# Optimization experiments

Hardware: AMD Instinct MI355X
Metric: run time of the kernel (lower is better)

The kernel has to match this reference:

```python
import jax, jax.numpy as jnp
import numpy as np

N, C, NUM_IDS = 4096, 2048, 256


def setup_inputs() -> dict:
    key = jax.random.key(0)
    k1, k2 = jax.random.split(key)
    x = jax.random.normal(k1, (N, C), dtype=jnp.float32)
    target = jax.random.randint(k2, (N,), 0, NUM_IDS, dtype=jnp.int64)
    return {
        "input": x,
        "target": target,
        "hyper_paramter": 1,
        "usemean": 1,
        "use_exp": 0,
    }


def _pair_stats(x, W):
    """Vectorized sum over lower-tri pairs (i>j) weighted by W (lower-triangular 0/1).

    cov = sum_{i>j} W_ij (x_i - x_j)(x_i - x_j)^T = X^T (diag(S 1) - S) X, S = W + W^T
    vec = sum_{i>j} W_ij (x_i - x_j)       = X^T (rowsum(W) - colsum(W))
    """
    S = W + W.T                       # [N, N] symmetric pair mask
    d = S.sum(axis=1)                 # degree
    Lx = d[:, None] * x - S @ x       # (diag(d) - S) @ X, [N, C]
    cov = x.T @ Lx                    # [C, C]
    vec = x.T @ (W.sum(axis=1) - W.sum(axis=0))  # [C]
    return cov, vec, W.sum()


def reference(input, target, hyper_paramter, usemean, use_exp):
    x = input
    same_id = (target[:, None] == target[None, :])
    pos_l = jnp.tril(same_id.astype(x.dtype), -1)          # positive pairs, i>j
    neg_l = jnp.tril((~same_id).astype(x.dtype), -1)       # negative pairs, i>j

    cov_i, sum_i, npos = _pair_stats(x, pos_l)
    cov_j, sum_j, nneg = _pair_stats(x, neg_l)

    norm_i = jnp.linalg.norm(cov_i)
    norm_j = jnp.linalg.norm(cov_j)

    if use_exp:
        dist = jnp.exp(-jnp.linalg.norm(cov_i - cov_j))
        loss = dist
    else:
        # original broadcasts zeros(C) + diff(C,1) -> (C,C) matrix of identical
        # columns; its Frobenius norm = sqrt(C) * norm(column vector)
        mean_norm = jnp.sqrt(jnp.asarray(x.shape[1], x.dtype)) * jnp.linalg.norm(
            sum_i / npos - sum_j / nneg
        )
        dist = norm_i - hyper_paramter * norm_j - usemean * mean_norm
        loss = jnp.maximum(dist, 0.0)
    return (loss, dist, norm_i, norm_j)
```

## Files before the change

### kernel.cpp

```cpp
#include <hip/hip_runtime.h>
#include <math.h>


#define N_ROWS 4096
#define C_DIM  2048
#define NCLS   256
#define RLCAP  96
#define NRB    17
#define NKS    64
#define TSB    16384
#define SLOT_B 32768

typedef __attribute__((ext_vector_type(8))) short short8v;
typedef __attribute__((ext_vector_type(4))) float f32x4;

__device__ __forceinline__ unsigned short f2bf(float f) {
    unsigned u = __float_as_uint(f);
    u += 0x7FFF + ((u >> 16) & 1);
    return (unsigned short)(u >> 16);
}

__device__ __forceinline__ void gload16(const void* g, void* l) {
    __builtin_amdgcn_global_load_lds(
        (const __attribute__((address_space(1))) unsigned int*)g,
        (__attribute__((address_space(3))) unsigned int*)l, 16, 0, 0);
}

__device__ __forceinline__ int swz_off(int r, int c8) {
    return r * 64 + ((c8 ^ ((r >> 1) & 3)) << 4);
}

__global__ __launch_bounds__(256) void k_scan_conv(
    const int* __restrict__ t, const float* __restrict__ x,
    float* __restrict__ ca, float* __restrict__ cb,
    float* __restrict__ dr, float* __restrict__ nposf,
    unsigned char* __restrict__ xbf) {
    __shared__ int ts[N_ROWS];
    __shared__ int rl[RLCAP];
    __shared__ int cnt_s;
    int a = blockIdx.x, tid = threadIdx.x;
    for (int i = tid; i < N_ROWS; i += 256) ts[i] = t[i];
    __syncthreads();
    if (tid < 64) {
        int lane = tid;
        unsigned long long ltmask = (1ULL << lane) - 1ULL;
        int base = 0;
        for (int i0 = 0; i0 < N_ROWS; i0 += 64) {
            int i = i0 + lane;
            bool m = (ts[i] == a);
            unsigned long long mask = __ballot(m);
            if (m) {
                int r = base + (int)__popcll(mask & ltmask);
                if (r < RLCAP) rl[r] = i;
            }
            base += (int)__popcll(mask);
        }
        if (lane == 0) {
            cnt_s = base;
            float cf = (float)base;
            atomicAdd(nposf, 0.5f * cf * (cf - 1.f));
        }
        int cc = base < RLCAP ? base : RLCAP;
        for (int r = lane; r < cc; r += 64) {
            int i = rl[r];
            ca[i] = (float)(2 * r - base + 1);
            cb[i] = (float)(2 * i - 2 * r + base - N_ROWS);
            dr[i] = (float)base;
        }
    }
    __syncthreads();
    int cnt = cnt_s < RLCAP ? cnt_s : RLCAP;
    int c0 = tid * 4, c1 = 1024 + tid * 4;
    float s0=0,s1=0,s2=0,s3=0,s4=0,s5=0,s6=0,s7=0;
    int ks0 = c0 >> 5, c80 = (c0 & 31) >> 3, sb0 = (c0 & 4) << 1;
    int ks1 = c1 >> 5, c81 = (c1 & 31) >> 3, sb1 = (c1 & 4) << 1;
    for (int r = 0; r < cnt; ++r) {
        int i = rl[r];
        const float* row = x + (size_t)i * C_DIM;
        float4 v0 = *(const float4*)(row + c0);
        float4 v1 = *(const float4*)(row + c1);
        s0+=v0.x; s1+=v0.y; s2+=v0.z; s3+=v0.w;
        s4+=v1.x; s5+=v1.y; s6+=v1.z; s7+=v1.w;
        int rb2 = i >> 8, rr = i & 255;
        unsigned char* tb = xbf + (size_t)rb2 * NKS * TSB;
        int2 w0, w1;
        w0.x = (int)((unsigned)f2bf(v0.x) | ((unsigned)f2bf(v0.y) << 16));
        w0.y = (int)((unsigned)f2bf(v0.z) | ((unsigned)f2bf(v0.w) << 16));
        w1.x = (int)((unsigned)f2bf(v1.x) | ((unsigned)f2bf(v1.y) << 16));
        w1.y = (int)((unsigned)f2bf(v1.z) | ((unsigned)f2bf(v1.w) << 16));
        *(int2*)(tb + (size_t)ks0 * TSB + swz_off(rr, c80) + sb0) = w0;
        *(int2*)(tb + (size_t)ks1 * TSB + swz_off(rr, c81) + sb1) = w1;
    }
    unsigned char* tbg = xbf + (size_t)16 * NKS * TSB;
    int2 g0, g1;
    g0.x = (int)((unsigned)f2bf(s0) | ((unsigned)f2bf(s1) << 16));
    g0.y = (int)((unsigned)f2bf(s2) | ((unsigned)f2bf(s3) << 16));
    g1.x = (int)((unsigned)f2bf(s4) | ((unsigned)f2bf(s5) << 16));
    g1.y = (int)((unsigned)f2bf(s6) | ((unsigned)f2bf(s7) << 16));
    *(int2*)(tbg + (size_t)ks0 * TSB + swz_off(a, c80) + sb0) = g0;
    *(int2*)(tbg + (size_t)ks1 * TSB + swz_off(a, c81) + sb1) = g1;
}

__device__ __forceinline__ short8v frag64(const unsigned char* buf, int row0,
                                          int lane) {
    int r = row0 + (lane & 15);
    int c8 = lane >> 4;
    return *(const short8v*)(buf + swz_off(r, c8));
}

__global__ __launch_bounds__(1024, 4) void k_gram(
    const unsigned char* __restrict__ xbf, const float* __restrict__ dr,
    const float* __restrict__ ca, const float* __restrict__ cb,
    const float* __restrict__ nposf, float* __restrict__ ssq) {
    const int nwg = NRB * (NRB + 1) / 2;
    int orig = blockIdx.x;
    int q8 = nwg >> 3, r8 = nwg & 7;
    int xcd = orig & 7, loc = orig >> 3;
    int b = (xcd < r8 ? xcd * (q8 + 1) : r8 * (q8 + 1) + (xcd - r8) * q8) + loc;
    int bi = 0;
    while (b >= NRB - bi) { b -= NRB - bi; ++bi; }
    int bj = bi + b;
    bool diag = (bi == bj);
    bool needRS = (bj == NRB - 1);

    __shared__ __align__(16) unsigned char Sl[4][SLOT_B];
    __shared__ float drow[256], dcol[256], urow[256], ucol[256];
    __shared__ float rsum[256];
    __shared__ float wred[16 * 16];

    int tid = threadIdx.x;
    int lane = tid & 63;
    int w = tid >> 6;
    int wr4 = w >> 2;
    int wc4 = w & 3;

    const unsigned char* abase = xbf + (size_t)bi * NKS * TSB;
    const unsigned char* bbase = xbf + (size_t)bj * NKS * TSB;
    int off0 = w * 1024 + lane * 16;

#pragma unroll
    for (int p = 0; p < 2; ++p) {
        gload16(abase + (size_t)p * TSB + off0, Sl[p] + off0);
        gload16(bbase + (size_t)p * TSB + off0, Sl[p] + 16384 + off0);
    }
    if (tid < 256) {
        float np = nposf[0];
        float inp = 1.f / np;
        float inn = 1.f / (0.5f * (float)N_ROWS * ((float)N_ROWS - 1.f) - np);
        int gi = bi * 256 + tid;
        bool vi = gi < N_ROWS;
        drow[tid] = vi ? dr[gi] : 0.f;
        urow[tid] = vi ? (ca[gi] * inp - cb[gi] * inn) : 0.f;
        int gj = bj * 256 + tid;
        bool vj = gj < N_ROWS;
        dcol[tid] = vj ? dr[gj] : 0.f;
        ucol[tid] = vj ? (ca[gj] * inp - cb[gj] * inn) : 0.f;
        rsum[tid] = 0.f;
    }

    f32x4 acc[4][4] = {};
    __syncthreads();

#define STAGE_STEP(ks)                                                         \
    {                                                                          \
        unsigned char* sl = Sl[(ks) & 3];                                      \
        gload16(abase + (size_t)(ks) * TSB + off0, sl + off0);                 \
        gload16(bbase + (size_t)(ks) * TSB + off0, sl + 16384 + off0);         \
    }

#define COMPUTE_STEP(t)                                                        \
    {                                                                          \
        const unsigned char* sb = Sl[(t) & 3];                                 \
        short8v A[4], B[4];                                                    \
        _Pragma("unroll")                                                      \
        for (int m = 0; m < 4; ++m) A[m] = frag64(sb, wr4 * 64 + m * 16, lane);\
        _Pragma("unroll")                                                      \
        for (int n = 0; n < 4; ++n) B[n] = frag64(sb + 16384, wc4 * 64 + n * 16, lane);\
        __builtin_amdgcn_s_setprio(1);                                         \
        _Pragma("unroll")                                                      \
        for (int m = 0; m < 4; ++m)                                            \
            _Pragma("unroll")                                                  \
            for (int n = 0; n < 4; ++n)                                        \
                acc[m][n] = __builtin_amdgcn_mfma_f32_16x16x32_bf16(           \
                    A[m], B[n], acc[m][n], 0, 0, 0);                           \
        __builtin_amdgcn_s_setprio(0);                                         \
    }

    for (int t = 0; t < NKS - 2; ++t) {
        STAGE_STEP(t + 2);
        asm volatile("s_waitcnt vmcnt(4)" ::: "memory");
        asm volatile("s_barrier" ::: "memory");
        COMPUTE_STEP(t);
    }
    asm volatile("s_waitcnt vmcnt(2)" ::: "memory");
    asm volatile("s_barrier" ::: "memory");
    COMPUTE_STEP(NKS - 2);
    asm volatile("s_waitcnt vmcnt(0)" ::: "memory");
    asm volatile("s_barrier" ::: "memory");
    COMPUTE_STEP(NKS - 1);

    float fK = diag ? 1.f : 2.f;
    float vs[7] = {0,0,0,0,0,0,0};
#pragma unroll
    for (int m = 0; m < 4; ++m) {
#pragma unroll
        for (int qq = 0; qq < 4; ++qq) {
            int iw = wr4 * 64 + m * 16 + (lane >> 4) * 4 + qq;
            int gi = bi * 256 + iw;
            float di = drow[iw];
            float ui = urow[iw];
            bool iX = gi < N_ROWS;
            float rs = 0.f;
#pragma unroll
            for (int n = 0; n < 4; ++n) {
                int jw = wc4 * 64 + n * 16 + (lane & 15);
                int gj = bj * 256 + jw;
                float dj = dcol[jw];
                float k = acc[m][n][qq];
                float k2 = k * k;
                bool jX = gj < N_ROWS;
                if (iX && jX) {
                    vs[0] += fK * k2;
                    vs[1] += 0.5f * fK * (di + dj) * k2;
                    vs[2] += fK * di * dj * k2;
                    vs[6] += fK * ui * ucol[jw] * k;
                } else if (iX) {
                    vs[3] += k2;
                    vs[4] += di * k2;
                } else if (!jX) {
                    vs[5] += fK * k2;
                }
                if (needRS) rs += k;
            }
            if (needRS) {
                rs += __shfl_xor(rs, 1);
                rs += __shfl_xor(rs, 2);
                rs += __shfl_xor(rs, 4);
                rs += __shfl_xor(rs, 8);
                if ((lane & 15) == 0) atomicAdd(&rsum[iw], rs);
            }
        }
    }
#pragma unroll
    for (int v = 0; v < 7; ++v) {
        float xv = vs[v];
        for (int off = 32; off; off >>= 1) xv += __shfl_down(xv, off);
        if (lane == 0) wred[w * 16 + v] = xv;
    }
    __syncthreads();
    if (tid < 7) {
        float sum = 0.f;
#pragma unroll
        for (int ww = 0; ww < 16; ++ww) sum += wred[ww * 16 + tid];
        atomicAdd(ssq + (tid == 6 ? 10 : tid), sum);
    }
    if (needRS && tid < 256) {
        float r = rsum[tid];
        float a6 = diag ? 0.f : r * r;
        float a7 = diag ? 0.f : drow[tid] * r * r;
        float a8 = diag ? r * r : 0.f;
        float a9 = diag ? r : 0.f;
        for (int off = 32; off; off >>= 1) {
            a6 += __shfl_down(a6, off);
            a7 += __shfl_down(a7, off);
            a8 += __shfl_down(a8, off);
            a9 += __shfl_down(a9, off);
        }
        if (lane == 0) {
            atomicAdd(ssq + 6, a6);
            atomicAdd(ssq + 7, a7);
            atomicAdd(ssq + 8, a8);
            atomicAdd(ssq + 9, a9);
        }
    }
#undef STAGE_STEP
#undef COMPUTE_STEP
}

__global__ void k_final(const float* __restrict__ ssq, const float* __restrict__ nposf,
                        const int* __restrict__ hyper, const int* __restrict__ usemean,
                        const int* __restrict__ use_exp, float* __restrict__ out) {
    if (threadIdx.x != 0) return;
    double S0 = ssq[0], S1 = ssq[1], S2 = ssq[2], R2 = ssq[3], PG = ssq[4];
    double Q2 = ssq[5], TS = ssq[6], PS = ssq[7], GS = ssq[8], SS = ssq[9];
    double U2 = ssq[10];
    double Nf = (double)N_ROWS;
    double ni2 = S2 - 2.0 * PG + Q2;
    double nj2 = Nf * Nf * S0 + S2 + SS * SS + Q2 - 2.0 * Nf * S1
               - 2.0 * Nf * TS + 2.0 * Nf * R2 + 2.0 * PS - 2.0 * PG - 2.0 * GS;
    double trAB = Nf * S1 - S2 - PS + 2.0 * PG - Nf * R2 + GS - Q2;
    double d2 = ni2 - 2.0 * trAB + nj2;
    float norm_i = (float)sqrt(fmax(ni2, 0.0));
    float norm_j = (float)sqrt(fmax(nj2, 0.0));
    float h = (float)hyper[0], um = (float)usemean[0];
    float loss, dist;
    if (use_exp[0]) {
        dist = (float)exp(-sqrt(fmax(d2, 0.0)));
        loss = dist;
    } else {
        float mean_norm = sqrtf((float)C_DIM) * sqrtf(fmaxf((float)U2, 0.f));
        dist = norm_i - h * norm_j - um * mean_norm;
        loss = fmaxf(dist, 0.f);
    }
    out[0] = loss; out[1] = dist; out[2] = norm_i; out[3] = norm_j;
}

extern "C" void kernel_launch(void* const* d_in, const int* in_sizes, int n_in,
                              void* d_out, int out_size, void* d_ws, size_t ws_size,
                              hipStream_t stream) {
    const float* x = (const float*)d_in[0];
    const int* t = (const int*)d_in[1];
    const int* hyper = (const int*)d_in[2];
    const int* usemean = (const int*)d_in[3];
    const int* use_exp = (const int*)d_in[4];
    float* out = (float*)d_out;

    unsigned char* xbf = (unsigned char*)d_ws;
    size_t xbf_bytes = (size_t)NRB * NKS * TSB;
    float* ca    = (float*)(xbf + xbf_bytes);
    float* cb    = ca + N_ROWS;
    float* dr    = cb + N_ROWS;
    float* ssq   = dr + N_ROWS;
    float* nposf = ssq + 16;

    hipMemsetAsync(ssq, 0, 32 * sizeof(float), stream);

    k_scan_conv<<<NCLS, 256, 0, stream>>>(t, x, ca, cb, dr, nposf, xbf);
    k_gram<<<NRB * (NRB + 1) / 2, 1024, 0, stream>>>(xbf, dr, ca, cb, nposf, ssq);
    k_final<<<1, 64, 0, stream>>>(ssq, nposf, hyper, usemean, use_exp, out);
}
```

Baseline: 86.90 us.

## Switch Gram matmul operands from bf16 to fp8 MFMA with new swizzled layout

Converts the staged input rows and group sums to packed fp8 instead of bf16. This halves the bytes per element, so each 16KB tile now covers 64 columns and the K-step count drops from 64 to 32. The MFMA inner loop uses fp8 16x16x32 instructions, two per K-slice, and a new 8-byte XOR swizzle for LDS fragment loads. It cuts memory traffic and may raise MFMA throughput, at the cost of much lower precision in the covariance norms.

```diff
diff --git a/kernel.cpp b/kernel.cpp
--- a/kernel.cpp
+++ b/kernel.cpp
@@ -7,18 +7,11 @@
 #define NCLS   256
 #define RLCAP  96
 #define NRB    17
-#define NKS    64
+#define NKS    32
 #define TSB    16384
 #define SLOT_B 32768
 
-typedef __attribute__((ext_vector_type(8))) short short8v;
 typedef __attribute__((ext_vector_type(4))) float f32x4;
-
-__device__ __forceinline__ unsigned short f2bf(float f) {
-    unsigned u = __float_as_uint(f);
-    u += 0x7FFF + ((u >> 16) & 1);
-    return (unsigned short)(u >> 16);
-}
 
 __device__ __forceinline__ void gload16(const void* g, void* l) {
     __builtin_amdgcn_global_load_lds(
@@ -26,8 +19,10 @@
         (__attribute__((address_space(3))) unsigned int*)l, 16, 0, 0);
 }
 
-__device__ __forceinline__ int swz_off(int r, int c8) {
-    return r * 64 + ((c8 ^ ((r >> 1) & 3)) << 4);
+__device__ __forceinline__ int pk4_fp8(float a, float b, float c, float d) {
+    int r = __builtin_amdgcn_cvt_pk_fp8_f32(a, b, 0, false);
+    r = __builtin_amdgcn_cvt_pk_fp8_f32(c, d, r, true);
+    return r;
 }
 
 __global__ __launch_bounds__(256) void k_scan_conv(
@@ -72,8 +67,8 @@
     int cnt = cnt_s < RLCAP ? cnt_s : RLCAP;
     int c0 = tid * 4, c1 = 1024 + tid * 4;
     float s0=0,s1=0,s2=0,s3=0,s4=0,s5=0,s6=0,s7=0;
-    int ks0 = c0 >> 5, c80 = (c0 & 31) >> 3, sb0 = (c0 & 4) << 1;
-    int ks1 = c1 >> 5, c81 = (c1 & 31) >> 3, sb1 = (c1 & 4) << 1;
+    int ks0 = c0 >> 6, sl0 = (c0 & 63) >> 3, hf0 = (c0 >> 2) & 1;
+    int ks1 = c1 >> 6, sl1 = (c1 & 63) >> 3, hf1 = (c1 >> 2) & 1;
     for (int r = 0; r < cnt; ++r) {
         int i = rl[r];
         const float* row = x + (size_t)i * C_DIM;
@@ -83,29 +78,23 @@
         s4+=v1.x; s5+=v1.y; s6+=v1.z; s7+=v1.w;
         int rb2 = i >> 8, rr = i & 255;
         unsigned char* tb = xbf + (size_t)rb2 * NKS * TSB;
-        int2 w0, w1;
-        w0.x = (int)((unsigned)f2bf(v0.x) | ((unsigned)f2bf(v0.y) << 16));
-        w0.y = (int)((unsigned)f2bf(v0.z) | ((unsigned)f2bf(v0.w) << 16));
-        w1.x = (int)((unsigned)f2bf(v1.x) | ((unsigned)f2bf(v1.y) << 16));
-        w1.y = (int)((unsigned)f2bf(v1.z) | ((unsigned)f2bf(v1.w) << 16));
-        *(int2*)(tb + (size_t)ks0 * TSB + swz_off(rr, c80) + sb0) = w0;
-        *(int2*)(tb + (size_t)ks1 * TSB + swz_off(rr, c81) + sb1) = w1;
+        int w0 = pk4_fp8(v0.x, v0.y, v0.z, v0.w);
+        int w1 = pk4_fp8(v1.x, v1.y, v1.z, v1.w);
+        *(int*)(tb + (size_t)ks0 * TSB + rr * 64 + ((sl0 ^ (rr & 7)) << 3) + hf0 * 4) = w0;
+        *(int*)(tb + (size_t)ks1 * TSB + rr * 64 + ((sl1 ^ (rr & 7)) << 3) + hf1 * 4) = w1;
     }
     unsigned char* tbg = xbf + (size_t)16 * NKS * TSB;
-    int2 g0, g1;
-    g0.x = (int)((unsigned)f2bf(s0) | ((unsigned)f2bf(s1) << 16));
-    g0.y = (int)((unsigned)f2bf(s2) | ((unsigned)f2bf(s3) << 16));
-    g1.x = (int)((unsigned)f2bf(s4) | ((unsigned)f2bf(s5) << 16));
-    g1.y = (int)((unsigned)f2bf(s6) | ((unsigned)f2bf(s7) << 16));
-    *(int2*)(tbg + (size_t)ks0 * TSB + swz_off(a, c80) + sb0) = g0;
-    *(int2*)(tbg + (size_t)ks1 * TSB + swz_off(a, c81) + sb1) = g1;
-}
-
-__device__ __forceinline__ short8v frag64(const unsigned char* buf, int row0,
-                                          int lane) {
+    int g0 = pk4_fp8(s0, s1, s2, s3);
+    int g1 = pk4_fp8(s4, s5, s6, s7);
+    *(int*)(tbg + (size_t)ks0 * TSB + a * 64 + ((sl0 ^ (a & 7)) << 3) + hf0 * 4) = g0;
+    *(int*)(tbg + (size_t)ks1 * TSB + a * 64 + ((sl1 ^ (a & 7)) << 3) + hf1 * 4) = g1;
+}
+
+__device__ __forceinline__ long frag8(const unsigned char* buf, int row0,
+                                      int ch, int lane) {
     int r = row0 + (lane & 15);
-    int c8 = lane >> 4;
-    return *(const short8v*)(buf + swz_off(r, c8));
+    int slot = ch * 4 + (lane >> 4);
+    return *(const long*)(buf + r * 64 + ((slot ^ (r & 7)) << 3));
 }
 
 __global__ __launch_bounds__(1024, 4) void k_gram(
@@ -171,18 +160,27 @@
 #define COMPUTE_STEP(t)                                                        \
     {                                                                          \
         const unsigned char* sb = Sl[(t) & 3];                                 \
-        short8v A[4], B[4];                                                    \
+        long A0[4], A1[4], B0[4], B1[4];                                       \
         _Pragma("unroll")                                                      \
-        for (int m = 0; m < 4; ++m) A[m] = frag64(sb, wr4 * 64 + m * 16, lane);\
+        for (int m = 0; m < 4; ++m) {                                          \
+            A0[m] = frag8(sb, wr4 * 64 + m * 16, 0, lane);                     \
+            A1[m] = frag8(sb, wr4 * 64 + m * 16, 1, lane);                     \
+        }                                                                      \
         _Pragma("unroll")                                                      \
-        for (int n = 0; n < 4; ++n) B[n] = frag64(sb + 16384, wc4 * 64 + n * 16, lane);\
+        for (int n = 0; n < 4; ++n) {                                          \
+            B0[n] = frag8(sb + 16384, wc4 * 64 + n * 16, 0, lane);             \
+            B1[n] = frag8(sb + 16384, wc4 * 64 + n * 16, 1, lane);             \
+        }                                                                      \
         __builtin_amdgcn_s_setprio(1);                                         \
         _Pragma("unroll")                                                      \
         for (int m = 0; m < 4; ++m)                                            \
             _Pragma("unroll")                                                  \
-            for (int n = 0; n < 4; ++n)                                        \
-                acc[m][n] = __builtin_amdgcn_mfma_f32_16x16x32_bf16(           \
-                    A[m], B[n], acc[m][n], 0, 0, 0);                           \
+            for (int n = 0; n < 4; ++n) {                                      \
+                acc[m][n] = __builtin_amdgcn_mfma_f32_16x16x32_fp8_fp8(        \
+                    A0[m], B0[n], acc[m][n], 0, 0, 0);                         \
+                acc[m][n] = __builtin_amdgcn_mfma_f32_16x16x32_fp8_fp8(        \
+                    A1[m], B1[n], acc[m][n], 0, 0, 0);                         \
+            }                                                                  \
         __builtin_amdgcn_s_setprio(0);                                         \
     }
 
```

New measurement: 83.54 us. 1.04x faster.
